# Kernel optimization log

Hardware: AMD Instinct MI355X
Metric: run time of the kernel (lower is better)

Reference implementation:

```python
import jax, jax.numpy as jnp
import numpy as np

GAMMA = 1.0
BIG = 1e8  # boundary sentinel, matches 100000000.0 in the original


def _softdtw_R(D, gamma=GAMMA):
    """Forward soft-DTW DP. D: [N, M] distance matrix -> R: [N, M].
    R[i,j] = D[i,j] + softmin_gamma(R[i-1,j-1], R[i-1,j], R[i,j-1])."""
    N, M = D.shape
    dt = D.dtype

    def row_step(prev_row, d_row):
        # prev_row: [M+1] = padded previous row R[i-1, 0..M] (index 0 = left boundary)
        diag = prev_row[:-1]  # R[i-1, j-1]
        up = prev_row[1:]     # R[i-1, j]

        def cell(r_left, xs):
            dg, u, d = xs
            z = jnp.stack([dg, u, r_left]) * (-1.0 / gamma)
            m = jnp.max(z)
            softmin = -gamma * (jnp.log(jnp.sum(jnp.exp(z - m))) + m)
            r = d + softmin
            return r, r

        _, row = jax.lax.scan(cell, jnp.asarray(BIG, dt), (diag, up, d_row))
        new_prev = jnp.concatenate([jnp.full((1,), BIG, dt), row])
        return new_prev, row

    # padded row 0: corner R[0,0]=0, top boundary = BIG
    init = jnp.concatenate([jnp.zeros((1,), dt), jnp.full((M,), BIG, dt)])
    _, R = jax.lax.scan(row_step, init, D)
    return R  # [N, M]


def reference(x):
    # x: [B, N, M, 1] batch of distance matrices
    D = jnp.squeeze(x, axis=-1)
    R = jax.vmap(_softdtw_R)(D)
    return R[..., None]  # [B, N, M, 1]


def setup_inputs() -> dict:
    key = jax.random.key(0)
    B, N, M = 32, 512, 512
    x = jax.random.uniform(key, (B, N, M, 1), dtype=jnp.float32)
    return {"x": x}
```

## Files before the change

kernel.cpp:

```cpp
#include <hip/hip_runtime.h>

#define N_DIM 512
#define M_DIM 512
#define NQUAD 128
#define TSTEPS 192
#define DEPTH 4
#define SLOT_BYTES 8192
#define RING_BYTES (DEPTH * SLOT_BYTES)
#define SIGMA_MAX (TSTEPS + DEPTH)
#define BSTRIDE (N_DIM * M_DIM)
#define GSTRIDE (NQUAD * 64)
#define DSKEW_B ((size_t)SIGMA_MAX * SLOT_BYTES)
#define ESKEW_B ((size_t)TSTEPS * SLOT_BYTES)
#define ROW_BYTES 2048
#define ROW_MAX (511 * 2048)
#define LN2F 0.6931471805599453f

#define AS1 __attribute__((address_space(1)))
#define AS3 __attribute__((address_space(3)))

__global__ __launch_bounds__(256) void skew_pre(const float* __restrict__ D,
                                                char* __restrict__ Dsk) {
    const int b  = blockIdx.y;
    const int t0 = blockIdx.x << 3;
    __shared__ float4 tile[4096];
    const int tid = threadIdx.x;

    const float4* src = (const float4*)(D + (size_t)b * BSTRIDE) + ((size_t)t0 << 9);
    #pragma unroll
    for (int w = 0; w < 16; ++w) {
        const int idx = (w << 8) + tid;
        const float4 v = src[idx];
        tile[idx] = make_float4(__expf(-v.x), __expf(-v.y), __expf(-v.z), __expf(-v.w));
    }
    __syncthreads();

    char* dst = Dsk + (size_t)b * DSKEW_B;
    #pragma unroll
    for (int w = 0; w < 18; ++w) {
        const int w2 = (w << 8) + tid;
        const int li = w2 & 7;
        const int ch = (w2 >> 3) & 7;
        const int si = w2 >> 6;
        const int lmin = max(0, si - 7);
        const int l = lmin + li;
        if (si < 71 && l <= min(63, si)) {
            const int ti = si - l;
            const int k = ch >> 1, h = ch & 1;
            const float4 val = tile[(((ti << 2) + k) << 7) + (l << 1) + h];
            *(float4*)(dst + (size_t)(t0 + si) * SLOT_BYTES + (ch << 10) + (l << 4)) = val;
        }
    }
}

__global__ __launch_bounds__(256) void unskew_post(const char* __restrict__ Esk,
                                                   const float* __restrict__ gm,
                                                   float* __restrict__ R) {
    const int b  = blockIdx.y;
    const int t0 = blockIdx.x << 3;
    __shared__ float4 tile[4096];
    const int tid = threadIdx.x;

    const char* srcE = Esk + (size_t)b * ESKEW_B;
    #pragma unroll
    for (int w = 0; w < 18; ++w) {
        const int w2 = (w << 8) + tid;
        const int li = w2 & 7;
        const int ch = (w2 >> 3) & 7;
        const int si = w2 >> 6;
        const int lmin = max(0, si - 7);
        const int l = lmin + li;
        if (si < 71 && l <= min(63, si)) {
            const int ti = si - l;
            const int k = ch >> 1, h = ch & 1;
            const float4 val = *(const float4*)(srcE + (size_t)(t0 + si) * SLOT_BYTES
                                                + (ch << 10) + (l << 4));
            tile[(((ti << 2) + k) << 7) + (l << 1) + h] = val;
        }
    }
    __syncthreads();

    float* dstR = R + (size_t)b * BSTRIDE;
    const float* gmb = gm + b * GSTRIDE;
    #pragma unroll
    for (int w = 0; w < 16; ++w) {
        const int idx = (w << 8) + tid;
        const int rit = idx >> 7;
        const int c4  = idx & 127;
        const int tq  = t0 + (rit >> 2);
        const float g = gmb[(tq << 6) + (c4 >> 1)];
        const float4 v = tile[idx];
        *(float4*)(dstR + (((size_t)(t0 << 2) + rit) << 9) + (c4 << 2)) =
            make_float4(g - __logf(v.x), g - __logf(v.y), g - __logf(v.z), g - __logf(v.w));
    }
}

__global__ __launch_bounds__(256) void log_post_plain(float4* __restrict__ E4,
                                                      const float* __restrict__ gm, int n4) {
    int i = blockIdx.x * blockDim.x + threadIdx.x;
    const int stride = gridDim.x * blockDim.x;
    for (; i < n4; i += stride) {
        const int b   = i >> 16;
        const int rem = i & 65535;
        const int row = rem >> 7;
        const int c4  = rem & 127;
        const float g = gm[(b << 13) + ((row >> 2) << 6) + (c4 >> 1)];
        const float4 v = E4[i];
        E4[i] = make_float4(g - __logf(v.x), g - __logf(v.y),
                            g - __logf(v.z), g - __logf(v.w));
    }
}

__device__ inline float shup1(float x) {
    int r = __builtin_amdgcn_update_dpp(0, __float_as_int(x), 0x138, 0xf, 0xf, true);
    return __int_as_float(r);
}
__device__ inline int shup1i(int x) {
    return __builtin_amdgcn_update_dpp(0, x, 0x138, 0xf, 0xf, true);
}
__device__ inline int fr_exp(float x) {
    int e; asm("v_frexp_exp_i32_f32 %0, %1" : "=v"(e) : "v"(x)); return e;
}
__device__ inline float ldx(float x, int k) {
    float r; asm("v_ldexp_f32 %0, %1, %2" : "=v"(r) : "v"(x), "v"(k)); return r;
}

__global__ __launch_bounds__(64, 1) void softdtw_dp_skew(const char* __restrict__ Dsk,
                                                         char* __restrict__ Esk,
                                                         float* __restrict__ gmap) {
    const int b = blockIdx.x;
    const int l = threadIdx.x;
    const int laneB16 = l << 4;

    const char* __restrict__ DskB = Dsk + (size_t)b * DSKEW_B;
    char*       __restrict__ EskB = Esk + (size_t)b * ESKEW_B;
    float*      __restrict__ gm   = gmap + (size_t)b * GSTRIDE;

    __shared__ char ring[RING_BYTES] __attribute__((aligned(16)));
    const unsigned ring_base = (unsigned)(size_t)(AS3 char*)ring;

    float Ep[8];
    #pragma unroll
    for (int k = 0; k < 8; ++k) Ep[k] = 0.0f;
    float fQ = 0.0f;
    int   KG = 0, KE = 0, Kh = 0;
    float expA7 = 0.0f, expB7 = 0.0f, expC7 = 0.0f, expD7 = 0.0f;
    float E7hD = 0.0f;

    int dsk_off = DEPTH * SLOT_BYTES;
    int es_off  = 0;

    float4 P[8], Nx[8];
    #pragma unroll
    for (int ch = 0; ch < 8; ++ch)
        P[ch] = *(const float4*)(DskB + ch * 1024 + laneB16);
    #pragma unroll
    for (int sig = 1; sig < DEPTH; ++sig) {
        const char* gp = DskB + sig * SLOT_BYTES + laneB16;
        #pragma unroll
        for (int ch = 0; ch < 8; ++ch)
            __builtin_amdgcn_global_load_lds((const AS1 void*)(gp + ch * 1024),
                                             (AS3 void*)(ring + sig * SLOT_BYTES + ch * 1024),
                                             16, 0, 0);
    }
    asm volatile("s_waitcnt vmcnt(0)" ::: "memory");

    auto rowfma = [&](const float* endv, float eLeft, const float* Q, float* E) {
        float e = eLeft;
        #pragma unroll
        for (int c = 0; c < 8; ++c) {
            e = __builtin_fmaf(endv[c], e, endv[c] * Q[c]);
            E[c] = e;
        }
    };

    auto step = [&](int s, float4 (&cur)[8], float4 (&nxt)[8]) {
        {
            const unsigned wo = ((unsigned)s & (DEPTH - 1)) * SLOT_BYTES;
            const char* gp = DskB + dsk_off + laneB16;
            #pragma unroll
            for (int ch = 0; ch < 8; ++ch)
                __builtin_amdgcn_global_load_lds((const AS1 void*)(gp + ch * 1024),
                                                 (AS3 void*)(ring + wo + ch * 1024), 16, 0, 0);
            dsk_off += SLOT_BYTES;
        }
        asm volatile("s_waitcnt vmcnt(51)" ::: "memory");

        const float E7sA = shup1(expA7);
        const float E7sB = shup1(expB7);
        const float E7sC = shup1(expC7);
        const float E7sD = shup1(expD7);
        const int   Ks   = shup1i(KE);

        const unsigned raddr = ring_base
                             + (unsigned)((s + 1) & (DEPTH - 1)) * SLOT_BYTES
                             + (unsigned)laneB16;
        asm volatile("ds_read_b128 %0, %8 offset:0\n\t"
                     "ds_read_b128 %1, %8 offset:1024\n\t"
                     "ds_read_b128 %2, %8 offset:2048\n\t"
                     "ds_read_b128 %3, %8 offset:3072\n\t"
                     "ds_read_b128 %4, %8 offset:4096\n\t"
                     "ds_read_b128 %5, %8 offset:5120\n\t"
                     "ds_read_b128 %6, %8 offset:6144\n\t"
                     "ds_read_b128 %7, %8 offset:7168"
                     : "=&v"(nxt[0]), "=&v"(nxt[1]), "=&v"(nxt[2]), "=&v"(nxt[3]),
                       "=&v"(nxt[4]), "=&v"(nxt[5]), "=&v"(nxt[6]), "=&v"(nxt[7])
                     : "v"(raddr));

        asm volatile("s_waitcnt lgkmcnt(8)" ::: "memory");
        __builtin_amdgcn_sched_barrier(0);

        const int t = s - l;
        if (t >= 0 && t < NQUAD) {
            const float endA[8] = {cur[0].x, cur[0].y, cur[0].z, cur[0].w,
                                   cur[1].x, cur[1].y, cur[1].z, cur[1].w};
            const float endB[8] = {cur[2].x, cur[2].y, cur[2].z, cur[2].w,
                                   cur[3].x, cur[3].y, cur[3].z, cur[3].w};
            const float endC[8] = {cur[4].x, cur[4].y, cur[4].z, cur[4].w,
                                   cur[5].x, cur[5].y, cur[5].z, cur[5].w};
            const float endD[8] = {cur[6].x, cur[6].y, cur[6].z, cur[6].w,
                                   cur[7].x, cur[7].y, cur[7].z, cur[7].w};

            const bool is0    = (t == 0);
            const bool origin = is0 && (l == 0);
            int K = is0 ? (Ks - fr_exp(E7sA)) : KG;
            K = origin ? 0 : K;
            const float fq = is0 ? 0.0f : fQ;
            const int dKs = K - Ks;
            const int dKh = K - Kh;

            const float eLA = ldx(E7sA, dKs);
            const float eLB = ldx(E7sB, dKs);
            const float eLC = ldx(E7sC, dKs);
            const float eLD = ldx(E7sD, dKs);
            float eDA0 = ldx(E7hD, dKh);
            eDA0 = is0 ? 0.0f : eDA0;
            eDA0 = origin ? 1.0f : eDA0;

            float QA[8];
            QA[0] = eDA0 + fq * Ep[0];
            #pragma unroll
            for (int c = 1; c < 8; ++c) QA[c] = fq * (Ep[c - 1] + Ep[c]);
            float EA[8];
            rowfma(endA, eLA, QA, EA);

            float QB[8];
            QB[0] = eLA + EA[0];
            #pragma unroll
            for (int c = 1; c < 8; ++c) QB[c] = EA[c - 1] + EA[c];
            float EB[8];
            rowfma(endB, eLB, QB, EB);

            float QC[8];
            QC[0] = eLB + EB[0];
            #pragma unroll
            for (int c = 1; c < 8; ++c) QC[c] = EB[c - 1] + EB[c];
            float EC[8];
            rowfma(endC, eLC, QC, EC);

            float QD[8];
            QD[0] = eLC + EC[0];
            #pragma unroll
            for (int c = 1; c < 8; ++c) QD[c] = EC[c - 1] + EC[c];
            float ED[8];
            rowfma(endD, eLD, QD, ED);

            char* sb  = EskB + es_off + laneB16;
            char* sb2 = sb + 4096;
            *(float4*)(sb)         = make_float4(EA[0], EA[1], EA[2], EA[3]);
            *(float4*)(sb + 1024)  = make_float4(EA[4], EA[5], EA[6], EA[7]);
            *(float4*)(sb + 2048)  = make_float4(EB[0], EB[1], EB[2], EB[3]);
            *(float4*)(sb + 3072)  = make_float4(EB[4], EB[5], EB[6], EB[7]);
            *(float4*)(sb2)        = make_float4(EC[0], EC[1], EC[2], EC[3]);
            *(float4*)(sb2 + 1024) = make_float4(EC[4], EC[5], EC[6], EC[7]);
            *(float4*)(sb2 + 2048) = make_float4(ED[0], ED[1], ED[2], ED[3]);
            *(float4*)(sb2 + 3072) = make_float4(ED[4], ED[5], ED[6], ED[7]);
            gm[(t << 6) + l] = (float)K * LN2F;

            const int ed = fr_exp(ED[0]);
            KG = K - ed;
            fQ = ldx(1.0f, -ed);
            KE = K;
            #pragma unroll
            for (int c = 0; c < 8; ++c) Ep[c] = ED[c];
            expA7 = EA[7]; expB7 = EB[7]; expC7 = EC[7]; expD7 = ED[7];
        }

        E7hD = E7sD;
        Kh   = Ks;
        es_off += SLOT_BYTES;
    };

    for (int s = 0; s < TSTEPS; s += 2) {
        step(s,     P,  Nx);
        step(s + 1, Nx, P);
    }
}

__global__ __launch_bounds__(64, 1) void softdtw_dp_direct(const float* __restrict__ Dsrc,
                                                           float* __restrict__ Eout,
                                                           float* __restrict__ gmap) {
    const int b     = blockIdx.x;
    const int l     = threadIdx.x;
    const int laneB = l << 5;
    const float* __restrict__ Db = Dsrc + (size_t)b * BSTRIDE;
    float*       __restrict__ Rb = Eout + (size_t)b * BSTRIDE;
    float*       __restrict__ gm = gmap + (size_t)b * GSTRIDE;
    __shared__ char ring[RING_BYTES] __attribute__((aligned(16)));
    const unsigned ring_base = (unsigned)(size_t)(AS3 char*)ring;

    float Ep[8];
    #pragma unroll
    for (int k = 0; k < 8; ++k) Ep[k] = 0.0f;
    float fQ = 0.0f;
    int KG = 0, KE = 0, Kh = 0;
    float expA7 = 0.0f, expB7 = 0.0f, expC7 = 0.0f, expD7 = 0.0f;
    float E7hD = 0.0f;
    int raw[4];
    #pragma unroll
    for (int k = 0; k < 4; ++k) raw[k] = (16 + k) * ROW_BYTES - (l << 13);
    int soff = -(l << 13);

    float4 P[8], Nx[8];
    #pragma unroll
    for (int row = 0; row < 4; ++row) {
        const int r = min(max(-4 * l + row, 0), N_DIM - 1);
        P[2 * row]     = *(const float4*)(Db + (size_t)r * M_DIM + (l << 3));
        P[2 * row + 1] = *(const float4*)(Db + (size_t)r * M_DIM + (l << 3) + 4);
    }
    #pragma unroll
    for (int sig = 1; sig < DEPTH; ++sig) {
        const unsigned wo = (unsigned)sig * SLOT_BYTES;
        #pragma unroll
        for (int k = 0; k < 4; ++k) {
            const int cl = min(max((4 * (sig - l) + k) * ROW_BYTES, 0), ROW_MAX);
            const char* gp = (const char*)Db + cl + laneB;
            __builtin_amdgcn_global_load_lds((const AS1 void*)gp,
                                             (AS3 void*)(ring + wo + (2 * k) * 1024), 16, 0, 0);
            __builtin_amdgcn_global_load_lds((const AS1 void*)(gp + 16),
                                             (AS3 void*)(ring + wo + (2 * k + 1) * 1024), 16, 0, 0);
        }
    }
    asm volatile("s_waitcnt vmcnt(0)" ::: "memory");

    auto rowfma = [&](const float* endv, float eLeft, const float* Q, float* E) {
        float e = eLeft;
        #pragma unroll
        for (int c = 0; c < 8; ++c) {
            e = __builtin_fmaf(endv[c], e, endv[c] * Q[c]);
            E[c] = e;
        }
    };

    auto step = [&](int s, float4 (&cur)[8], float4 (&nxt)[8]) {
        {
            const unsigned wo = ((unsigned)(s + DEPTH) & (DEPTH - 1)) * SLOT_BYTES;
            #pragma unroll
            for (int k = 0; k < 4; ++k) {
                const int cl = min(max(raw[k], 0), ROW_MAX);
                const char* gp = (const char*)Db + cl + laneB;
                __builtin_amdgcn_global_load_lds((const AS1 void*)gp,
                                                 (AS3 void*)(ring + wo + (2 * k) * 1024), 16, 0, 0);
                __builtin_amdgcn_global_load_lds((const AS1 void*)(gp + 16),
                                                 (AS3 void*)(ring + wo + (2 * k + 1) * 1024), 16, 0, 0);
                raw[k] += 4 * ROW_BYTES;
            }
        }
        asm volatile("s_waitcnt vmcnt(51)" ::: "memory");
        const float E7sA = shup1(expA7);
        const float E7sB = shup1(expB7);
        const float E7sC = shup1(expC7);
        const float E7sD = shup1(expD7);
        const int   Ks   = shup1i(KE);
        const unsigned raddr = ring_base
                             + (unsigned)((s + 1) & (DEPTH - 1)) * SLOT_BYTES
                             + (unsigned)l * 16u;
        asm volatile("ds_read_b128 %0, %8 offset:0\n\t"
                     "ds_read_b128 %1, %8 offset:1024\n\t"
                     "ds_read_b128 %2, %8 offset:2048\n\t"
                     "ds_read_b128 %3, %8 offset:3072\n\t"
                     "ds_read_b128 %4, %8 offset:4096\n\t"
                     "ds_read_b128 %5, %8 offset:5120\n\t"
                     "ds_read_b128 %6, %8 offset:6144\n\t"
                     "ds_read_b128 %7, %8 offset:7168"
                     : "=&v"(nxt[0]), "=&v"(nxt[1]), "=&v"(nxt[2]), "=&v"(nxt[3]),
                       "=&v"(nxt[4]), "=&v"(nxt[5]), "=&v"(nxt[6]), "=&v"(nxt[7])
                     : "v"(raddr));
        asm volatile("s_waitcnt lgkmcnt(8)" ::: "memory");
        __builtin_amdgcn_sched_barrier(0);
        const int t = s - l;
        if (t >= 0 && t < NQUAD) {
            const float endA[8] = {__expf(-cur[0].x), __expf(-cur[0].y), __expf(-cur[0].z), __expf(-cur[0].w),
                                   __expf(-cur[1].x), __expf(-cur[1].y), __expf(-cur[1].z), __expf(-cur[1].w)};
            const float endB[8] = {__expf(-cur[2].x), __expf(-cur[2].y), __expf(-cur[2].z), __expf(-cur[2].w),
                                   __expf(-cur[3].x), __expf(-cur[3].y), __expf(-cur[3].z), __expf(-cur[3].w)};
            const float endC[8] = {__expf(-cur[4].x), __expf(-cur[4].y), __expf(-cur[4].z), __expf(-cur[4].w),
                                   __expf(-cur[5].x), __expf(-cur[5].y), __expf(-cur[5].z), __expf(-cur[5].w)};
            const float endD[8] = {__expf(-cur[6].x), __expf(-cur[6].y), __expf(-cur[6].z), __expf(-cur[6].w),
                                   __expf(-cur[7].x), __expf(-cur[7].y), __expf(-cur[7].z), __expf(-cur[7].w)};
            const bool is0    = (t == 0);
            const bool origin = is0 && (l == 0);
            int K = is0 ? (Ks - fr_exp(E7sA)) : KG;
            K = origin ? 0 : K;
            const float fq = is0 ? 0.0f : fQ;
            const int dKs = K - Ks;
            const int dKh = K - Kh;
            const float eLA = ldx(E7sA, dKs);
            const float eLB = ldx(E7sB, dKs);
            const float eLC = ldx(E7sC, dKs);
            const float eLD = ldx(E7sD, dKs);
            float eDA0 = ldx(E7hD, dKh);
            eDA0 = is0 ? 0.0f : eDA0;
            eDA0 = origin ? 1.0f : eDA0;
            float QA[8];
            QA[0] = eDA0 + fq * Ep[0];
            #pragma unroll
            for (int c = 1; c < 8; ++c) QA[c] = fq * (Ep[c - 1] + Ep[c]);
            float EA[8]; rowfma(endA, eLA, QA, EA);
            float QB[8];
            QB[0] = eLA + EA[0];
            #pragma unroll
            for (int c = 1; c < 8; ++c) QB[c] = EA[c - 1] + EA[c];
            float EB[8]; rowfma(endB, eLB, QB, EB);
            float QC[8];
            QC[0] = eLB + EB[0];
            #pragma unroll
            for (int c = 1; c < 8; ++c) QC[c] = EB[c - 1] + EB[c];
            float EC[8]; rowfma(endC, eLC, QC, EC);
            float QD[8];
            QD[0] = eLC + EC[0];
            #pragma unroll
            for (int c = 1; c < 8; ++c) QD[c] = EC[c - 1] + EC[c];
            float ED[8]; rowfma(endD, eLD, QD, ED);
            char* sb  = (char*)Rb + soff + laneB;
            char* sb2 = sb + 4096;
            *(float4*)(sb)         = make_float4(EA[0], EA[1], EA[2], EA[3]);
            *(float4*)(sb + 16)    = make_float4(EA[4], EA[5], EA[6], EA[7]);
            *(float4*)(sb + 2048)  = make_float4(EB[0], EB[1], EB[2], EB[3]);
            *(float4*)(sb + 2064)  = make_float4(EB[4], EB[5], EB[6], EB[7]);
            *(float4*)(sb2)        = make_float4(EC[0], EC[1], EC[2], EC[3]);
            *(float4*)(sb2 + 16)   = make_float4(EC[4], EC[5], EC[6], EC[7]);
            *(float4*)(sb2 + 2048) = make_float4(ED[0], ED[1], ED[2], ED[3]);
            *(float4*)(sb2 + 2064) = make_float4(ED[4], ED[5], ED[6], ED[7]);
            gm[(t << 6) + l] = (float)K * LN2F;
            const int ed = fr_exp(ED[0]);
            KG = K - ed;
            fQ = ldx(1.0f, -ed);
            KE = K;
            #pragma unroll
            for (int c = 0; c < 8; ++c) Ep[c] = ED[c];
            expA7 = EA[7]; expB7 = EB[7]; expC7 = EC[7]; expD7 = ED[7];
        }
        E7hD = E7sD;
        Kh   = Ks;
        soff += 4 * ROW_BYTES;
    };

    for (int s = 0; s < TSTEPS; s += 2) {
        step(s,     P,  Nx);
        step(s + 1, Nx, P);
    }
}

extern "C" void kernel_launch(void* const* d_in, const int* in_sizes, int n_in,
                              void* d_out, int out_size, void* d_ws, size_t ws_size,
                              hipStream_t stream) {
    const float* x = (const float*)d_in[0];
    float* out     = (float*)d_out;
    const int B    = in_sizes[0] / BSTRIDE;
    const size_t GMAP_BYTES = (size_t)B * GSTRIDE * sizeof(float);
    const size_t need_skew  = (size_t)B * (DSKEW_B + ESKEW_B) + GMAP_BYTES;

    if (ws_size >= need_skew) {
        char*  dsk = (char*)d_ws;
        char*  esk = dsk + (size_t)B * DSKEW_B;
        float* gm  = (float*)(esk + (size_t)B * ESKEW_B);
        skew_pre<<<dim3(16, B), dim3(256), 0, stream>>>(x, dsk);
        softdtw_dp_skew<<<dim3(B), dim3(64), 0, stream>>>(dsk, esk, gm);
        unskew_post<<<dim3(16, B), dim3(256), 0, stream>>>(esk, gm, out);
    } else {
        float* gm = (float*)d_ws;
        const int n4 = (B * BSTRIDE) / 4;
        softdtw_dp_direct<<<dim3(B), dim3(64), 0, stream>>>(x, out, gm);
        log_post_plain<<<dim3(2048), dim3(256), 0, stream>>>((float4*)out, gm, n4);
    }
}
```

Baseline: 123.6 us.

## Store skewed exp-distances and DP results as bf16 with eight-row octet tiles

The skewed intermediate buffers for exp(-D) and the DP results are now packed as bf16 pairs instead of fp32. This halves the bytes moved through global memory and the LDS ring per slot. Each lane now processes eight rows per wavefront step instead of four, so the diagonal schedule shrinks from 192 to 128 steps and per-step overhead is amortised, while each step's serial FMA chain doubles. The pre- and post-processing kernels are retiled to match. Storing intermediates in bf16 loses precision, which could affect accuracy after the final log.

```diff
diff --git a/kernel.cpp b/kernel.cpp
--- a/kernel.cpp
+++ b/kernel.cpp
@@ -2,31 +2,41 @@
 
 #define N_DIM 512
 #define M_DIM 512
-#define NQUAD 128
-#define TSTEPS 192
+#define NOCT 64
+#define TSTEPS 128
+#define SLOT8 8192
+#define DDEPTH 4
+#define RING8 (DDEPTH * SLOT8)
+#define SIGMA_MAX (TSTEPS + DDEPTH)
+#define BSTRIDE (N_DIM * M_DIM)
+#define GSTR_O (NOCT * 64)
+#define GSTR_Q (128 * 64)
+#define DSKEW_B ((size_t)SIGMA_MAX * SLOT8)
+#define ESKEW_B ((size_t)TSTEPS * SLOT8)
+#define LN2F 0.6931471805599453f
 #define DEPTH 4
 #define SLOT_BYTES 8192
 #define RING_BYTES (DEPTH * SLOT_BYTES)
-#define SIGMA_MAX (TSTEPS + DEPTH)
-#define BSTRIDE (N_DIM * M_DIM)
-#define GSTRIDE (NQUAD * 64)
-#define DSKEW_B ((size_t)SIGMA_MAX * SLOT_BYTES)
-#define ESKEW_B ((size_t)TSTEPS * SLOT_BYTES)
 #define ROW_BYTES 2048
 #define ROW_MAX (511 * 2048)
-#define LN2F 0.6931471805599453f
 
 #define AS1 __attribute__((address_space(1)))
 #define AS3 __attribute__((address_space(3)))
+
+__device__ inline unsigned pkbf16(float lo, float hi) {
+    unsigned r; asm("v_cvt_pk_bf16_f32 %0, %1, %2" : "=v"(r) : "v"(lo), "v"(hi)); return r;
+}
+__device__ inline float ubf_lo(unsigned u) { return __int_as_float((int)(u << 16)); }
+__device__ inline float ubf_hi(unsigned u) { return __int_as_float((int)(u & 0xffff0000u)); }
 
 __global__ __launch_bounds__(256) void skew_pre(const float* __restrict__ D,
                                                 char* __restrict__ Dsk) {
     const int b  = blockIdx.y;
-    const int t0 = blockIdx.x << 3;
+    const int t0 = blockIdx.x << 2;
     __shared__ float4 tile[4096];
     const int tid = threadIdx.x;
 
-    const float4* src = (const float4*)(D + (size_t)b * BSTRIDE) + ((size_t)t0 << 9);
+    const float4* src = (const float4*)(D + (size_t)b * BSTRIDE) + ((size_t)t0 << 10);
     #pragma unroll
     for (int w = 0; w < 16; ++w) {
         const int idx = (w << 8) + tid;
@@ -37,18 +47,22 @@
 
     char* dst = Dsk + (size_t)b * DSKEW_B;
     #pragma unroll
-    for (int w = 0; w < 18; ++w) {
+    for (int w = 0; w < 9; ++w) {
         const int w2 = (w << 8) + tid;
-        const int li = w2 & 7;
-        const int ch = (w2 >> 3) & 7;
-        const int si = w2 >> 6;
-        const int lmin = max(0, si - 7);
+        const int li = w2 & 3;
+        const int ch = (w2 >> 2) & 7;
+        const int si = w2 >> 5;
+        const int lmin = max(0, si - 3);
         const int l = lmin + li;
-        if (si < 71 && l <= min(63, si)) {
+        if (si < 67 && l <= min(63, si)) {
             const int ti = si - l;
-            const int k = ch >> 1, h = ch & 1;
-            const float4 val = tile[(((ti << 2) + k) << 7) + (l << 1) + h];
-            *(float4*)(dst + (size_t)(t0 + si) * SLOT_BYTES + (ch << 10) + (l << 4)) = val;
+            const int base = (((ti << 3) + ch) << 7) + (l << 1);
+            const float4 a = tile[base];
+            const float4 c = tile[base + 1];
+            uint4 o;
+            o.x = pkbf16(a.x, a.y); o.y = pkbf16(a.z, a.w);
+            o.z = pkbf16(c.x, c.y); o.w = pkbf16(c.z, c.w);
+            *(uint4*)(dst + (size_t)(t0 + si) * SLOT8 + (ch << 10) + (l << 4)) = o;
         }
     }
 }
@@ -57,40 +71,41 @@
                                                    const float* __restrict__ gm,
                                                    float* __restrict__ R) {
     const int b  = blockIdx.y;
-    const int t0 = blockIdx.x << 3;
+    const int t0 = blockIdx.x << 2;
     __shared__ float4 tile[4096];
     const int tid = threadIdx.x;
 
     const char* srcE = Esk + (size_t)b * ESKEW_B;
     #pragma unroll
-    for (int w = 0; w < 18; ++w) {
+    for (int w = 0; w < 9; ++w) {
         const int w2 = (w << 8) + tid;
-        const int li = w2 & 7;
-        const int ch = (w2 >> 3) & 7;
-        const int si = w2 >> 6;
-        const int lmin = max(0, si - 7);
+        const int li = w2 & 3;
+        const int ch = (w2 >> 2) & 7;
+        const int si = w2 >> 5;
+        const int lmin = max(0, si - 3);
         const int l = lmin + li;
-        if (si < 71 && l <= min(63, si)) {
+        if (si < 67 && l <= min(63, si)) {
             const int ti = si - l;
-            const int k = ch >> 1, h = ch & 1;
-            const float4 val = *(const float4*)(srcE + (size_t)(t0 + si) * SLOT_BYTES
-                                                + (ch << 10) + (l << 4));
-            tile[(((ti << 2) + k) << 7) + (l << 1) + h] = val;
+            const uint4 v = *(const uint4*)(srcE + (size_t)(t0 + si) * SLOT8
+                                            + (ch << 10) + (l << 4));
+            const int base = (((ti << 3) + ch) << 7) + (l << 1);
+            tile[base]     = make_float4(ubf_lo(v.x), ubf_hi(v.x), ubf_lo(v.y), ubf_hi(v.y));
+            tile[base + 1] = make_float4(ubf_lo(v.z), ubf_hi(v.z), ubf_lo(v.w), ubf_hi(v.w));
         }
     }
     __syncthreads();
 
     float* dstR = R + (size_t)b * BSTRIDE;
-    const float* gmb = gm + b * GSTRIDE;
+    const float* gmb = gm + b * GSTR_O;
     #pragma unroll
     for (int w = 0; w < 16; ++w) {
         const int idx = (w << 8) + tid;
         const int rit = idx >> 7;
         const int c4  = idx & 127;
-        const int tq  = t0 + (rit >> 2);
-        const float g = gmb[(tq << 6) + (c4 >> 1)];
+        const int oc  = t0 + (rit >> 3);
+        const float g = gmb[(oc << 6) + (c4 >> 1)];
         const float4 v = tile[idx];
-        *(float4*)(dstR + (((size_t)(t0 << 2) + rit) << 9) + (c4 << 2)) =
+        *(float4*)(dstR + (((size_t)(t0 << 3) + rit) << 9) + (c4 << 2)) =
             make_float4(g - __logf(v.x), g - __logf(v.y), g - __logf(v.z), g - __logf(v.w));
     }
 }
@@ -134,9 +149,9 @@
 
     const char* __restrict__ DskB = Dsk + (size_t)b * DSKEW_B;
     char*       __restrict__ EskB = Esk + (size_t)b * ESKEW_B;
-    float*      __restrict__ gm   = gmap + (size_t)b * GSTRIDE;
-
-    __shared__ char ring[RING_BYTES] __attribute__((aligned(16)));
+    float*      __restrict__ gm   = gmap + (size_t)b * GSTR_O;
+
+    __shared__ char ring[RING8] __attribute__((aligned(16)));
     const unsigned ring_base = (unsigned)(size_t)(AS3 char*)ring;
 
     float Ep[8];
@@ -144,56 +159,71 @@
     for (int k = 0; k < 8; ++k) Ep[k] = 0.0f;
     float fQ = 0.0f;
     int   KG = 0, KE = 0, Kh = 0;
-    float expA7 = 0.0f, expB7 = 0.0f, expC7 = 0.0f, expD7 = 0.0f;
-    float E7hD = 0.0f;
-
-    int dsk_off = DEPTH * SLOT_BYTES;
+    float ex0 = 0.0f, ex1 = 0.0f, ex2 = 0.0f, ex3 = 0.0f;
+    float ex4 = 0.0f, ex5 = 0.0f, ex6 = 0.0f, ex7 = 0.0f;
+    float E7hH = 0.0f;
+
+    int dsk_off = DDEPTH * SLOT8;
     int es_off  = 0;
 
-    float4 P[8], Nx[8];
+    uint4 P[8], Nx[8];
     #pragma unroll
     for (int ch = 0; ch < 8; ++ch)
-        P[ch] = *(const float4*)(DskB + ch * 1024 + laneB16);
-    #pragma unroll
-    for (int sig = 1; sig < DEPTH; ++sig) {
-        const char* gp = DskB + sig * SLOT_BYTES + laneB16;
+        P[ch] = *(const uint4*)(DskB + ch * 1024 + laneB16);
+    #pragma unroll
+    for (int sig = 1; sig < DDEPTH; ++sig) {
+        const char* gp = DskB + sig * SLOT8 + laneB16;
         #pragma unroll
         for (int ch = 0; ch < 8; ++ch)
             __builtin_amdgcn_global_load_lds((const AS1 void*)(gp + ch * 1024),
-                                             (AS3 void*)(ring + sig * SLOT_BYTES + ch * 1024),
+                                             (AS3 void*)(ring + sig * SLOT8 + ch * 1024),
                                              16, 0, 0);
     }
     asm volatile("s_waitcnt vmcnt(0)" ::: "memory");
 
-    auto rowfma = [&](const float* endv, float eLeft, const float* Q, float* E) {
+    auto dorow = [&](const uint4 q, float eDiag, float eLeft,
+                     const float* Eprev, float* Eo) {
+        float end[8];
+        end[0] = ubf_lo(q.x); end[1] = ubf_hi(q.x);
+        end[2] = ubf_lo(q.y); end[3] = ubf_hi(q.y);
+        end[4] = ubf_lo(q.z); end[5] = ubf_hi(q.z);
+        end[6] = ubf_lo(q.w); end[7] = ubf_hi(q.w);
+        float Q[8];
+        Q[0] = eDiag + Eprev[0];
+        #pragma unroll
+        for (int c = 1; c < 8; ++c) Q[c] = Eprev[c - 1] + Eprev[c];
         float e = eLeft;
         #pragma unroll
         for (int c = 0; c < 8; ++c) {
-            e = __builtin_fmaf(endv[c], e, endv[c] * Q[c]);
-            E[c] = e;
+            e = __builtin_fmaf(end[c], e, end[c] * Q[c]);
+            Eo[c] = e;
         }
     };
 
-    auto step = [&](int s, float4 (&cur)[8], float4 (&nxt)[8]) {
+    auto step = [&](int s, uint4 (&cur)[8], uint4 (&nxt)[8]) {
         {
-            const unsigned wo = ((unsigned)s & (DEPTH - 1)) * SLOT_BYTES;
+            const unsigned wo = ((unsigned)s & (DDEPTH - 1)) * SLOT8;
             const char* gp = DskB + dsk_off + laneB16;
             #pragma unroll
             for (int ch = 0; ch < 8; ++ch)
                 __builtin_amdgcn_global_load_lds((const AS1 void*)(gp + ch * 1024),
                                                  (AS3 void*)(ring + wo + ch * 1024), 16, 0, 0);
-            dsk_off += SLOT_BYTES;
+            dsk_off += SLOT8;
         }
         asm volatile("s_waitcnt vmcnt(51)" ::: "memory");
 
-        const float E7sA = shup1(expA7);
-        const float E7sB = shup1(expB7);
-        const float E7sC = shup1(expC7);
-        const float E7sD = shup1(expD7);
+        const float E7s0 = shup1(ex0);
+        const float E7s1 = shup1(ex1);
+        const float E7s2 = shup1(ex2);
+        const float E7s3 = shup1(ex3);
+        const float E7s4 = shup1(ex4);
+        const float E7s5 = shup1(ex5);
+        const float E7s6 = shup1(ex6);
+        const float E7s7 = shup1(ex7);
         const int   Ks   = shup1i(KE);
 
         const unsigned raddr = ring_base
-                             + (unsigned)((s + 1) & (DEPTH - 1)) * SLOT_BYTES
+                             + (unsigned)((s + 1) & (DDEPTH - 1)) * SLOT8
                              + (unsigned)laneB16;
         asm volatile("ds_read_b128 %0, %8 offset:0\n\t"
                      "ds_read_b128 %1, %8 offset:1024\n\t"
@@ -211,84 +241,88 @@
         __builtin_amdgcn_sched_barrier(0);
 
         const int t = s - l;
-        if (t >= 0 && t < NQUAD) {
-            const float endA[8] = {cur[0].x, cur[0].y, cur[0].z, cur[0].w,
-                                   cur[1].x, cur[1].y, cur[1].z, cur[1].w};
-            const float endB[8] = {cur[2].x, cur[2].y, cur[2].z, cur[2].w,
-                                   cur[3].x, cur[3].y, cur[3].z, cur[3].w};
-            const float endC[8] = {cur[4].x, cur[4].y, cur[4].z, cur[4].w,
-                                   cur[5].x, cur[5].y, cur[5].z, cur[5].w};
-            const float endD[8] = {cur[6].x, cur[6].y, cur[6].z, cur[6].w,
-                                   cur[7].x, cur[7].y, cur[7].z, cur[7].w};
-
+        if (t >= 0 && t < NOCT) {
             const bool is0    = (t == 0);
             const bool origin = is0 && (l == 0);
-            int K = is0 ? (Ks - fr_exp(E7sA)) : KG;
+            int K = is0 ? (Ks - fr_exp(E7s0)) : KG;
             K = origin ? 0 : K;
             const float fq = is0 ? 0.0f : fQ;
             const int dKs = K - Ks;
             const int dKh = K - Kh;
 
-            const float eLA = ldx(E7sA, dKs);
-            const float eLB = ldx(E7sB, dKs);
-            const float eLC = ldx(E7sC, dKs);
-            const float eLD = ldx(E7sD, dKs);
-            float eDA0 = ldx(E7hD, dKh);
-            eDA0 = is0 ? 0.0f : eDA0;
-            eDA0 = origin ? 1.0f : eDA0;
-
-            float QA[8];
-            QA[0] = eDA0 + fq * Ep[0];
-            #pragma unroll
-            for (int c = 1; c < 8; ++c) QA[c] = fq * (Ep[c - 1] + Ep[c]);
-            float EA[8];
-            rowfma(endA, eLA, QA, EA);
-
-            float QB[8];
-            QB[0] = eLA + EA[0];
-            #pragma unroll
-            for (int c = 1; c < 8; ++c) QB[c] = EA[c - 1] + EA[c];
-            float EB[8];
-            rowfma(endB, eLB, QB, EB);
-
-            float QC[8];
-            QC[0] = eLB + EB[0];
-            #pragma unroll
-            for (int c = 1; c < 8; ++c) QC[c] = EB[c - 1] + EB[c];
-            float EC[8];
-            rowfma(endC, eLC, QC, EC);
-
-            float QD[8];
-            QD[0] = eLC + EC[0];
-            #pragma unroll
-            for (int c = 1; c < 8; ++c) QD[c] = EC[c - 1] + EC[c];
-            float ED[8];
-            rowfma(endD, eLD, QD, ED);
-
-            char* sb  = EskB + es_off + laneB16;
-            char* sb2 = sb + 4096;
-            *(float4*)(sb)         = make_float4(EA[0], EA[1], EA[2], EA[3]);
-            *(float4*)(sb + 1024)  = make_float4(EA[4], EA[5], EA[6], EA[7]);
-            *(float4*)(sb + 2048)  = make_float4(EB[0], EB[1], EB[2], EB[3]);
-            *(float4*)(sb + 3072)  = make_float4(EB[4], EB[5], EB[6], EB[7]);
-            *(float4*)(sb2)        = make_float4(EC[0], EC[1], EC[2], EC[3]);
-            *(float4*)(sb2 + 1024) = make_float4(EC[4], EC[5], EC[6], EC[7]);
-            *(float4*)(sb2 + 2048) = make_float4(ED[0], ED[1], ED[2], ED[3]);
-            *(float4*)(sb2 + 3072) = make_float4(ED[4], ED[5], ED[6], ED[7]);
+            const float eL0 = ldx(E7s0, dKs);
+            const float eL1 = ldx(E7s1, dKs);
+            const float eL2 = ldx(E7s2, dKs);
+            const float eL3 = ldx(E7s3, dKs);
+            const float eL4 = ldx(E7s4, dKs);
+            const float eL5 = ldx(E7s5, dKs);
+            const float eL6 = ldx(E7s6, dKs);
+            const float eL7 = ldx(E7s7, dKs);
+            float eD0 = ldx(E7hH, dKh);
+            eD0 = is0 ? 0.0f : eD0;
+            eD0 = origin ? 1.0f : eD0;
+
+            float Fp[8];
+            #pragma unroll
+            for (int c = 0; c < 8; ++c) Fp[c] = fq * Ep[c];
+
+            char* sb = EskB + es_off + laneB16;
+            float Ea[8], Eb[8];
+            uint4 o;
+
+            dorow(cur[0], eD0, eL0, Fp, Ea);
+            o.x = pkbf16(Ea[0], Ea[1]); o.y = pkbf16(Ea[2], Ea[3]);
+            o.z = pkbf16(Ea[4], Ea[5]); o.w = pkbf16(Ea[6], Ea[7]);
+            *(uint4*)(sb) = o;  ex0 = Ea[7];
+
+            dorow(cur[1], eL0, eL1, Ea, Eb);
+            o.x = pkbf16(Eb[0], Eb[1]); o.y = pkbf16(Eb[2], Eb[3]);
+            o.z = pkbf16(Eb[4], Eb[5]); o.w = pkbf16(Eb[6], Eb[7]);
+            *(uint4*)(sb + 1024) = o;  ex1 = Eb[7];
+
+            dorow(cur[2], eL1, eL2, Eb, Ea);
+            o.x = pkbf16(Ea[0], Ea[1]); o.y = pkbf16(Ea[2], Ea[3]);
+            o.z = pkbf16(Ea[4], Ea[5]); o.w = pkbf16(Ea[6], Ea[7]);
+            *(uint4*)(sb + 2048) = o;  ex2 = Ea[7];
+
+            dorow(cur[3], eL2, eL3, Ea, Eb);
+            o.x = pkbf16(Eb[0], Eb[1]); o.y = pkbf16(Eb[2], Eb[3]);
+            o.z = pkbf16(Eb[4], Eb[5]); o.w = pkbf16(Eb[6], Eb[7]);
+            *(uint4*)(sb + 3072) = o;  ex3 = Eb[7];
+
+            dorow(cur[4], eL3, eL4, Eb, Ea);
+            o.x = pkbf16(Ea[0], Ea[1]); o.y = pkbf16(Ea[2], Ea[3]);
+            o.z = pkbf16(Ea[4], Ea[5]); o.w = pkbf16(Ea[6], Ea[7]);
+            *(uint4*)(sb + 4096) = o;  ex4 = Ea[7];
+
+            dorow(cur[5], eL4, eL5, Ea, Eb);
+            o.x = pkbf16(Eb[0], Eb[1]); o.y = pkbf16(Eb[2], Eb[3]);
+            o.z = pkbf16(Eb[4], Eb[5]); o.w = pkbf16(Eb[6], Eb[7]);
+            *(uint4*)(sb + 5120) = o;  ex5 = Eb[7];
+
+            dorow(cur[6], eL5, eL6, Eb, Ea);
+            o.x = pkbf16(Ea[0], Ea[1]); o.y = pkbf16(Ea[2], Ea[3]);
+            o.z = pkbf16(Ea[4], Ea[5]); o.w = pkbf16(Ea[6], Ea[7]);
+            *(uint4*)(sb + 6144) = o;  ex6 = Ea[7];
+
+            dorow(cur[7], eL6, eL7, Ea, Eb);
+            o.x = pkbf16(Eb[0], Eb[1]); o.y = pkbf16(Eb[2], Eb[3]);
+            o.z = pkbf16(Eb[4], Eb[5]); o.w = pkbf16(Eb[6], Eb[7]);
+            *(uint4*)(sb + 7168) = o;  ex7 = Eb[7];
+
             gm[(t << 6) + l] = (float)K * LN2F;
 
-            const int ed = fr_exp(ED[0]);
+            const int ed = fr_exp(Eb[0]);
             KG = K - ed;
             fQ = ldx(1.0f, -ed);
             KE = K;
             #pragma unroll
-            for (int c = 0; c < 8; ++c) Ep[c] = ED[c];
-            expA7 = EA[7]; expB7 = EB[7]; expC7 = EC[7]; expD7 = ED[7];
-        }
-
-        E7hD = E7sD;
+            for (int c = 0; c < 8; ++c) Ep[c] = Eb[c];
+        }
+
+        E7hH = E7s7;
         Kh   = Ks;
-        es_off += SLOT_BYTES;
+        es_off += SLOT8;
     };
 
     for (int s = 0; s < TSTEPS; s += 2) {
@@ -305,7 +339,7 @@
     const int laneB = l << 5;
     const float* __restrict__ Db = Dsrc + (size_t)b * BSTRIDE;
     float*       __restrict__ Rb = Eout + (size_t)b * BSTRIDE;
-    float*       __restrict__ gm = gmap + (size_t)b * GSTRIDE;
+    float*       __restrict__ gm = gmap + (size_t)b * GSTR_Q;
     __shared__ char ring[RING_BYTES] __attribute__((aligned(16)));
     const unsigned ring_base = (unsigned)(size_t)(AS3 char*)ring;
 
@@ -389,7 +423,7 @@
         asm volatile("s_waitcnt lgkmcnt(8)" ::: "memory");
         __builtin_amdgcn_sched_barrier(0);
         const int t = s - l;
-        if (t >= 0 && t < NQUAD) {
+        if (t >= 0 && t < 128) {
             const float endA[8] = {__expf(-cur[0].x), __expf(-cur[0].y), __expf(-cur[0].z), __expf(-cur[0].w),
                                    __expf(-cur[1].x), __expf(-cur[1].y), __expf(-cur[1].z), __expf(-cur[1].w)};
             const float endB[8] = {__expf(-cur[2].x), __expf(-cur[2].y), __expf(-cur[2].z), __expf(-cur[2].w),
@@ -456,7 +490,7 @@
         soff += 4 * ROW_BYTES;
     };
 
-    for (int s = 0; s < TSTEPS; s += 2) {
+    for (int s = 0; s < 192; s += 2) {
         step(s,     P,  Nx);
         step(s + 1, Nx, P);
     }
@@ -468,7 +502,7 @@
     const float* x = (const float*)d_in[0];
     float* out     = (float*)d_out;
     const int B    = in_sizes[0] / BSTRIDE;
-    const size_t GMAP_BYTES = (size_t)B * GSTRIDE * sizeof(float);
+    const size_t GMAP_BYTES = (size_t)B * GSTR_O * sizeof(float);
     const size_t need_skew  = (size_t)B * (DSKEW_B + ESKEW_B) + GMAP_BYTES;
 
     if (ws_size >= need_skew) {
```

New measurement: 138.7 us. 1.12x slower.
